# Kernel optimization log

Hardware: AMD Instinct MI355X
Metric: run time of the kernel (lower is better)

## Reference

```python
import jax, jax.numpy as jnp
import numpy as np

D_MODEL = 768
D_STATE = 16
D_CONV = 4
EXPAND = 2
HEADDIM = 64
D_INNER = EXPAND * D_MODEL          # 1536
NHEADS = D_INNER // HEADDIM         # 24
CONV_DIM = D_INNER + 2 * D_STATE    # 1568
D_IN_PROJ = 2 * D_INNER + 2 * D_STATE + NHEADS  # 3128
BATCH, SEQ = 4, 2048


def _mamba_params(key, scale=0.02):
    ks = jax.random.split(key, 5)
    return dict(
        in_w=jax.random.normal(ks[0], (D_MODEL, D_IN_PROJ), jnp.float32) * scale,
        conv_w=jax.random.normal(ks[1], (CONV_DIM, D_CONV), jnp.float32) * scale,
        conv_b=jnp.zeros((CONV_DIM,), jnp.float32),
        dt_bias=jax.random.normal(ks[2], (NHEADS,), jnp.float32) * 0.1,
        A_log=jnp.log(jax.random.uniform(ks[3], (NHEADS,), jnp.float32, 1.0, 16.0)),
        D=jnp.ones((NHEADS,), jnp.float32),
        norm_w=jnp.ones((D_INNER,), jnp.float32),
        out_w=jax.random.normal(ks[4], (D_INNER, D_MODEL), jnp.float32) * scale,
    )


def setup_inputs() -> dict:
    key = jax.random.key(0)
    kx, kf, kb, k1, k2 = jax.random.split(key, 5)
    f = _mamba_params(kf)
    b = _mamba_params(kb)
    k1a, k1b = jax.random.split(k1)
    inp = {
        'x': jax.random.normal(kx, (BATCH, SEQ, D_MODEL), jnp.float32),
        'ln1_w': jnp.ones((D_MODEL,), jnp.float32), 'ln1_b': jnp.zeros((D_MODEL,), jnp.float32),
        'ln2_w': jnp.ones((D_MODEL,), jnp.float32), 'ln2_b': jnp.zeros((D_MODEL,), jnp.float32),
        'ffn_w1': jax.random.normal(k1a, (2 * D_MODEL, 4 * D_MODEL), jnp.float32) * 0.02,
        'ffn_b1': jnp.zeros((4 * D_MODEL,), jnp.float32),
        'ffn_w2': jax.random.normal(k1b, (4 * D_MODEL, D_MODEL), jnp.float32) * 0.02,
        'ffn_b2': jnp.zeros((D_MODEL,), jnp.float32),
    }
    for name, p in (('f', f), ('b', b)):
        for k, v in p.items():
            inp[name + '_' + k] = v
    return inp


def _layernorm(x, w, b, eps=1e-5):
    m = jnp.mean(x, -1, keepdims=True)
    v = jnp.mean((x - m) ** 2, -1, keepdims=True)
    return (x - m) * jax.lax.rsqrt(v + eps) * w + b


def _mamba2(u, in_w, conv_w, conv_b, dt_bias, A_log, D, norm_w, out_w):
    b, l, _ = u.shape
    zxbcdt = u @ in_w                               # (b,l,d_in_proj)
    z = zxbcdt[..., :D_INNER]
    xBC = zxbcdt[..., D_INNER:D_INNER + CONV_DIM]
    dt = jax.nn.softplus(zxbcdt[..., -NHEADS:] + dt_bias)   # (b,l,h)
    # depthwise causal conv1d (kernel D_CONV) + SiLU
    xpad = jnp.pad(xBC, ((0, 0), (D_CONV - 1, 0), (0, 0)))
    xc = sum(conv_w[:, k] * xpad[:, k:k + l, :] for k in range(D_CONV)) + conv_b
    xc = jax.nn.silu(xc)
    xh = xc[..., :D_INNER].reshape(b, l, NHEADS, HEADDIM)
    Bm = xc[..., D_INNER:D_INNER + D_STATE]          # (b,l,n), ngroups=1
    Cm = xc[..., D_INNER + D_STATE:]                 # (b,l,n)
    A = -jnp.exp(A_log)                              # (h,)
    dA = jnp.exp(dt * A)                             # (b,l,h)

    def step(h, inp):
        dA_t, dt_t, B_t, C_t, x_t = inp              # (b,h),(b,h),(b,n),(b,n),(b,h,p)
        h = h * dA_t[:, :, None, None] + (dt_t[:, :, None] * x_t)[..., None] * B_t[:, None, None, :]
        y = jnp.einsum('bhpn,bn->bhp', h, C_t)
        return h, y

    h0 = jnp.zeros((b, NHEADS, HEADDIM, D_STATE), u.dtype)
    xs = (dA.transpose(1, 0, 2), dt.transpose(1, 0, 2), Bm.transpose(1, 0, 2),
          Cm.transpose(1, 0, 2), xh.transpose(1, 0, 2, 3))
    _, ys = jax.lax.scan(step, h0, xs)               # ys: (l,b,h,p)
    y = ys.transpose(1, 0, 2, 3) + D[None, None, :, None] * xh
    y = y.reshape(b, l, D_INNER)
    # gated RMSNorm: rmsnorm(y * silu(z)) * weight
    yz = y * jax.nn.silu(z)
    yz = yz * jax.lax.rsqrt(jnp.mean(yz * yz, -1, keepdims=True) + 1e-5) * norm_w
    return yz @ out_w


def reference(x, ln1_w, ln1_b, ln2_w, ln2_b,
              f_in_w, f_conv_w, f_conv_b, f_dt_bias, f_A_log, f_D, f_norm_w, f_out_w,
              b_in_w, b_conv_w, b_conv_b, b_dt_bias, b_A_log, b_D, b_norm_w, b_out_w,
              ffn_w1, ffn_b1, ffn_w2, ffn_b2):
    xn = _layernorm(x, ln1_w, ln1_b)
    fo = _mamba2(xn, f_in_w, f_conv_w, f_conv_b, f_dt_bias, f_A_log, f_D, f_norm_w, f_out_w)
    bo = _mamba2(jnp.flip(xn, 1), b_in_w, b_conv_w, b_conv_b, b_dt_bias, b_A_log, b_D, b_norm_w, b_out_w)
    bo = jnp.flip(bo, 1)
    bi = jnp.concatenate([fo, bo], -1)
    h = jax.nn.gelu(bi @ ffn_w1 + ffn_b1, approximate=False)
    h = jax.nn.gelu(h @ ffn_w2 + ffn_b2, approximate=False)
    # dropout is identity in eval mode
    return _layernorm(x + h, ln2_w, ln2_b)
```

## Files before the change

### kernel.cpp

```cpp
#include <hip/hip_runtime.h>
#include <math.h>

#define BATCH   4
#define SEQ     2048
#define DMODEL  768
#define DSTATE  16
#define DCONV   4
#define HEADDIM 64
#define DINNER  1536
#define NHEADS  24
#define CONVDIM 1568
#define DINPROJ 3128
#define DFFN    3072
#define ROWS    (BATCH*SEQ)
#define QCH     128
#define NCHUNK  (SEQ/QCH)

typedef __attribute__((ext_vector_type(8))) short bhalf8;
typedef __attribute__((ext_vector_type(4))) float floatx4;

__device__ __forceinline__ float gelu_f(float x) {
    return 0.5f * x * (1.0f + erff(x * 0.70710678118654752f));
}

__device__ __forceinline__ void splitRNE(float v, unsigned short& h, unsigned short& l) {
    unsigned u = __float_as_uint(v);
    unsigned rr = u + 0x7FFFu + ((u >> 16) & 1u);
    unsigned short hi = (unsigned short)(rr >> 16);
    float rem = v - __uint_as_float(((unsigned)hi) << 16);
    unsigned u2 = __float_as_uint(rem);
    unsigned r2 = u2 + 0x7FFFu + ((u2 >> 16) & 1u);
    h = hi;
    l = (unsigned short)(r2 >> 16);
}

__device__ __forceinline__ void gl16(const unsigned short* g, unsigned short* l) {
    __builtin_amdgcn_global_load_lds(
        (const __attribute__((address_space(1))) void*)g,
        (__attribute__((address_space(3))) void*)l, 16, 0, 0);
}

__device__ __forceinline__ float2 blockReduce2(float a, float b) {
    #pragma unroll
    for (int o = 32; o > 0; o >>= 1) {
        a += __shfl_down(a, o, 64);
        b += __shfl_down(b, o, 64);
    }
    __shared__ float sa[4], sb[4];
    int w = threadIdx.x >> 6, lane = threadIdx.x & 63;
    if (lane == 0) { sa[w] = a; sb[w] = b; }
    __syncthreads();
    if (threadIdx.x == 0) {
        int nw = blockDim.x >> 6;
        for (int i = 1; i < nw; ++i) { a += sa[i]; b += sb[i]; }
        sa[0] = a; sb[0] = b;
    }
    __syncthreads();
    return make_float2(sa[0], sb[0]);
}

__global__ __launch_bounds__(256) void ln_kernel(
    const float* __restrict__ x, const float* __restrict__ res,
    const float* __restrict__ w, const float* __restrict__ b,
    float* __restrict__ out)
{
    int r = blockIdx.x;
    const float* xr = x + (size_t)r * DMODEL;
    float v[3]; float s = 0.f, ss = 0.f;
    #pragma unroll
    for (int i = 0; i < 3; ++i) {
        int c = threadIdx.x + i * 256;
        float t = xr[c];
        if (res) t += res[(size_t)r * DMODEL + c];
        v[i] = t; s += t; ss += t * t;
    }
    float2 red = blockReduce2(s, ss);
    float mean = red.x * (1.0f / DMODEL);
    float var  = red.y * (1.0f / DMODEL) - mean * mean;
    float inv  = rsqrtf(var + 1e-5f);
    #pragma unroll
    for (int i = 0; i < 3; ++i) {
        int c = threadIdx.x + i * 256;
        out[(size_t)r * DMODEL + c] = (v[i] - mean) * inv * w[c] + b[c];
    }
}

__global__ __launch_bounds__(256) void ln_split_kernel(
    const float* __restrict__ x,
    const float* __restrict__ w, const float* __restrict__ b,
    unsigned short* __restrict__ H, unsigned short* __restrict__ L)
{
    int r = blockIdx.x;
    const float* xr = x + (size_t)r * DMODEL;
    float v[3]; float s = 0.f, ss = 0.f;
    #pragma unroll
    for (int i = 0; i < 3; ++i) {
        int c = threadIdx.x + i * 256;
        float t = xr[c];
        v[i] = t; s += t; ss += t * t;
    }
    float2 red = blockReduce2(s, ss);
    float mean = red.x * (1.0f / DMODEL);
    float var  = red.y * (1.0f / DMODEL) - mean * mean;
    float inv  = rsqrtf(var + 1e-5f);
    #pragma unroll
    for (int i = 0; i < 3; ++i) {
        int c = threadIdx.x + i * 256;
        float o = (v[i] - mean) * inv * w[c] + b[c];
        unsigned short h, l;
        splitRNE(o, h, l);
        H[(size_t)r * DMODEL + c] = h;
        L[(size_t)r * DMODEL + c] = l;
    }
}

__global__ __launch_bounds__(256) void wconv(
    const float* __restrict__ W, unsigned short* __restrict__ TH,
    unsigned short* __restrict__ TL, int K, int N)
{
    __shared__ float t[32][33];
    int tx = threadIdx.x & 31, ty = threadIdx.x >> 5;
    int kb = blockIdx.y * 32, nb = blockIdx.x * 32;
    #pragma unroll
    for (int i = 0; i < 4; ++i) {
        int k = kb + ty + i * 8, n = nb + tx;
        t[ty + i * 8][tx] = (k < K && n < N) ? W[(size_t)k * N + n] : 0.f;
    }
    __syncthreads();
    #pragma unroll
    for (int i = 0; i < 4; ++i) {
        int n = nb + ty + i * 8, k = kb + tx;
        if (n < N && k < K) {
            unsigned short hi, lo;
            splitRNE(t[tx][ty + i * 8], hi, lo);
            TH[(size_t)n * K + k] = hi;
            TL[(size_t)n * K + k] = lo;
        }
    }
}

__global__ __launch_bounds__(256) void gemm3(
    const unsigned short* __restrict__ AHg, const unsigned short* __restrict__ ALg,
    const unsigned short* __restrict__ BHg, const unsigned short* __restrict__ BLg,
    float* __restrict__ C, unsigned short* __restrict__ CHo, unsigned short* __restrict__ CLo,
    const float* __restrict__ bias,
    int M, int N, int K, int ldc, int coloff,
    int revA, int revC, int act)
{
    (void)M;
    __shared__ __align__(16) unsigned short AsH[128 * 32], AsL[128 * 32];
    __shared__ __align__(16) unsigned short BsH[128 * 32], BsL[128 * 32];

    const int tid = threadIdx.x;
    const int m0 = blockIdx.y * 128;
    const int n0 = blockIdx.x * 128;

    size_t aoff[2], boff[2];
    int lofs[2];
    #pragma unroll
    for (int q = 0; q < 2; ++q) {
        int row = (tid >> 2) + 64 * q;
        int sd  = (tid & 3) ^ ((row >> 1) & 3);
        int ar = m0 + row;
        if (revA) ar = (ar & ~(SEQ - 1)) + (SEQ - 1 - (ar & (SEQ - 1)));
        aoff[q] = (size_t)ar * K + sd * 8;
        boff[q] = (size_t)(n0 + row) * K + sd * 8;
        lofs[q] = (tid + 256 * q) * 8;
    }

    auto stage = [&](int k0) {
        #pragma unroll
        for (int q = 0; q < 2; ++q) {
            gl16(AHg + aoff[q] + k0, AsH + lofs[q]);
            gl16(ALg + aoff[q] + k0, AsL + lofs[q]);
            gl16(BHg + boff[q] + k0, BsH + lofs[q]);
            gl16(BLg + boff[q] + k0, BsL + lofs[q]);
        }
    };

    auto frag = [&](const unsigned short* buf, int row, int slot) -> bhalf8 {
        int sp = slot ^ ((row >> 1) & 3);
        return *(const bhalf8*)(buf + row * 32 + sp * 8);
    };

    const int w = tid >> 6, lane = tid & 63;
    const int rw = (w >> 1) * 64, cw = (w & 1) * 64;
    const int lr = lane & 15;
    const int lq = lane >> 4;

    floatx4 acc[4][4];
    const floatx4 fz = {0.f, 0.f, 0.f, 0.f};
    #pragma unroll
    for (int i = 0; i < 4; ++i)
        #pragma unroll
        for (int j = 0; j < 4; ++j) acc[i][j] = fz;

    const int ktiles = K >> 5;
    stage(0);
    for (int kt = 0; kt < ktiles; ++kt) {
        __syncthreads();
        bhalf8 ah[4], al[4], bh[4], bl[4];
        #pragma unroll
        for (int i = 0; i < 4; ++i) {
            int ra = rw + i * 16 + lr;
            int rb = cw + i * 16 + lr;
            ah[i] = frag(AsH, ra, lq);
            al[i] = frag(AsL, ra, lq);
            bh[i] = frag(BsH, rb, lq);
            bl[i] = frag(BsL, rb, lq);
        }
        __syncthreads();
        if (kt + 1 < ktiles) stage((kt + 1) * 32);
        #pragma unroll
        for (int i = 0; i < 4; ++i)
            #pragma unroll
            for (int j = 0; j < 4; ++j) {
                acc[i][j] = __builtin_amdgcn_mfma_f32_16x16x32_bf16(ah[i], bh[j], acc[i][j], 0, 0, 0);
                acc[i][j] = __builtin_amdgcn_mfma_f32_16x16x32_bf16(ah[i], bl[j], acc[i][j], 0, 0, 0);
                acc[i][j] = __builtin_amdgcn_mfma_f32_16x16x32_bf16(al[i], bh[j], acc[i][j], 0, 0, 0);
            }
    }

    #pragma unroll
    for (int i = 0; i < 4; ++i) {
        #pragma unroll
        for (int j = 0; j < 4; ++j) {
            int gc = n0 + cw + j * 16 + lr;
            if (gc < N) {
                float bv = bias ? bias[gc] : 0.f;
                #pragma unroll
                for (int rg = 0; rg < 4; ++rg) {
                    int gm = m0 + rw + i * 16 + lq * 4 + rg;
                    if (revC) gm = (gm & ~(SEQ - 1)) + (SEQ - 1 - (gm & (SEQ - 1)));
                    float v = acc[i][j][rg] + bv;
                    if (act) v = gelu_f(v);
                    size_t o = (size_t)gm * ldc + coloff + gc;
                    if (CHo) {
                        unsigned short h, l;
                        splitRNE(v, h, l);
                        CHo[o] = h; CLo[o] = l;
                    } else {
                        C[o] = v;
                    }
                }
            }
        }
    }
}

__global__ __launch_bounds__(256) void conv_kernel(
    const float* __restrict__ zx, const float* __restrict__ cw,
    const float* __restrict__ cb, float* __restrict__ xcv,
    float* __restrict__ bc,
    const float* __restrict__ dt_bias, const float* __restrict__ A_log,
    float* __restrict__ dtda)
{
    int cg = blockIdx.x * 256 + threadIdx.x;
    int r = blockIdx.y;
    if (cg < CONVDIM / 4) {
        int c = cg * 4;
        int t = r & (SEQ - 1);
        int rb = r & ~(SEQ - 1);
        float4 acc = *(const float4*)&cb[c];
        #pragma unroll
        for (int k = 0; k < DCONV; ++k) {
            int tt = t - (DCONV - 1) + k;
            if (tt >= 0) {
                float4 xv = *(const float4*)&zx[(size_t)(rb + tt) * DINPROJ + DINNER + c];
                acc.x += cw[(c + 0) * DCONV + k] * xv.x;
                acc.y += cw[(c + 1) * DCONV + k] * xv.y;
                acc.z += cw[(c + 2) * DCONV + k] * xv.z;
                acc.w += cw[(c + 3) * DCONV + k] * xv.w;
            }
        }
        float4 v;
        v.x = acc.x / (1.0f + expf(-acc.x));
        v.y = acc.y / (1.0f + expf(-acc.y));
        v.z = acc.z / (1.0f + expf(-acc.z));
        v.w = acc.w / (1.0f + expf(-acc.w));
        if (c < DINNER) *(float4*)&xcv[(size_t)r * DINNER + c] = v;
        else            *(float4*)&bc[(size_t)r * 32 + (c - DINNER)] = v;
    } else if (cg >= CONVDIM / 4 && cg < CONVDIM / 4 + NHEADS / 4) {
        int h0 = (cg - CONVDIM / 4) * 4;
        float4 zv = *(const float4*)&zx[(size_t)r * DINPROJ + (DINPROJ - NHEADS) + h0];
        float zz[4] = {zv.x, zv.y, zv.z, zv.w};
        #pragma unroll
        for (int j = 0; j < 4; ++j) {
            int h = h0 + j;
            float v = zz[j] + dt_bias[h];
            float dt = (v > 20.f) ? v : log1pf(expf(v));
            float A = -expf(A_log[h]);
            float2 o = make_float2(dt, expf(dt * A));
            *(float2*)&dtda[(size_t)r * 48 + 2 * h] = o;
        }
    }
}

__global__ __launch_bounds__(64) void scan_a(
    const float* __restrict__ xcv, const float* __restrict__ bc,
    const float* __restrict__ dtda, const float* __restrict__ Dp,
    float* __restrict__ yout, float* __restrict__ S, float* __restrict__ cd)
{
    int blk = blockIdx.x;
    int bh = blk / NCHUNK, c = blk - bh * NCHUNK;
    int b = bh / NHEADS, h = bh - b * NHEADS;
    int p = threadIdx.x;
    float hs[DSTATE] = {};
    float Dv = Dp[h];
    float cum = 1.f;
    int t0 = c * QCH;
    for (int t = t0; t < t0 + QCH; ++t) {
        size_t r = (size_t)b * SEQ + t;
        float2 dd = *(const float2*)&dtda[r * 48 + 2 * h];
        float dt = dd.x;
        float dA = dd.y;
        float x  = xcv[r * DINNER + h * HEADDIM + p];
        cum *= dA;
        float coef = dt * x;
        const float* bcr = bc + r * 32;
        float y = 0.f;
        #pragma unroll
        for (int n = 0; n < DSTATE; ++n) {
            hs[n] = hs[n] * dA + coef * bcr[n];
            y += hs[n] * bcr[16 + n];
        }
        yout[r * DINPROJ + DINNER + h * HEADDIM + p] = y + Dv * x;
        if (p == 0) cd[r * NHEADS + h] = cum;
    }
    float* Sp = S + (((size_t)bh * NCHUNK + c) * HEADDIM + p) * DSTATE;
    #pragma unroll
    for (int n = 0; n < DSTATE; ++n) Sp[n] = hs[n];
}

__global__ __launch_bounds__(64) void scan_b(
    const float* __restrict__ cd, float* __restrict__ S)
{
    int bh = blockIdx.x;
    int b = bh / NHEADS, h = bh - b * NHEADS;
    int p = threadIdx.x;
    float H[DSTATE] = {};
    for (int c = 0; c < NCHUNK; ++c) {
        float* Sp = S + (((size_t)bh * NCHUNK + c) * HEADDIM + p) * DSTATE;
        float P = cd[((size_t)b * SEQ + c * QCH + QCH - 1) * NHEADS + h];
        float s[DSTATE];
        #pragma unroll
        for (int n = 0; n < DSTATE; ++n) s[n] = Sp[n];
        #pragma unroll
        for (int n = 0; n < DSTATE; ++n) Sp[n] = H[n];
        #pragma unroll
        for (int n = 0; n < DSTATE; ++n) H[n] = P * H[n] + s[n];
    }
}

__global__ __launch_bounds__(64) void scan_c(
    const float* __restrict__ bc, const float* __restrict__ cd,
    const float* __restrict__ S, float* __restrict__ yout)
{
    int blk = blockIdx.x;
    int bh = blk / (NCHUNK - 1), c = blk - bh * (NCHUNK - 1) + 1;
    int b = bh / NHEADS, h = bh - b * NHEADS;
    int p = threadIdx.x;
    const float* Hp = S + (((size_t)bh * NCHUNK + c) * HEADDIM + p) * DSTATE;
    float H[DSTATE];
    #pragma unroll
    for (int n = 0; n < DSTATE; ++n) H[n] = Hp[n];
    int t0 = c * QCH;
    for (int t = t0; t < t0 + QCH; ++t) {
        size_t r = (size_t)b * SEQ + t;
        const float* Cr = bc + r * 32 + 16;
        float dot = 0.f;
        #pragma unroll
        for (int n = 0; n < DSTATE; ++n) dot += H[n] * Cr[n];
        float cum = cd[r * NHEADS + h];
        yout[r * DINPROJ + DINNER + h * HEADDIM + p] += cum * dot;
    }
}

__global__ __launch_bounds__(256) void gnorm_kernel(
    const float* __restrict__ zx, const float* __restrict__ nw,
    unsigned short* __restrict__ H, unsigned short* __restrict__ L)
{
    int r = blockIdx.x;
    const float* zr = zx + (size_t)r * DINPROJ;
    float v[6]; float ss = 0.f;
    #pragma unroll
    for (int i = 0; i < 6; ++i) {
        int c = threadIdx.x + i * 256;
        float z = zr[c];
        float y = zr[DINNER + c];
        float t = y * z / (1.0f + expf(-z));
        v[i] = t; ss += t * t;
    }
    float2 red = blockReduce2(ss, 0.f);
    float sc = rsqrtf(red.x * (1.0f / DINNER) + 1e-5f);
    #pragma unroll
    for (int i = 0; i < 6; ++i) {
        int c = threadIdx.x + i * 256;
        float o = v[i] * sc * nw[c];
        unsigned short h, l;
        splitRNE(o, h, l);
        H[(size_t)r * DINNER + c] = h;
        L[(size_t)r * DINNER + c] = l;
    }
}

extern "C" void kernel_launch(void* const* d_in, const int* in_sizes, int n_in,
                              void* d_out, int out_size, void* d_ws, size_t ws_size,
                              hipStream_t stream)
{
    (void)in_sizes; (void)n_in; (void)out_size; (void)ws_size;
    const float* x     = (const float*)d_in[0];
    const float* ln1w  = (const float*)d_in[1];
    const float* ln1b  = (const float*)d_in[2];
    const float* ln2w  = (const float*)d_in[3];
    const float* ln2b  = (const float*)d_in[4];
    const float* ffnw1 = (const float*)d_in[5];
    const float* ffnb1 = (const float*)d_in[6];
    const float* ffnw2 = (const float*)d_in[7];
    const float* ffnb2 = (const float*)d_in[8];
    const float* p[2][8];
    for (int d = 0; d < 2; ++d)
        for (int i = 0; i < 8; ++i)
            p[d][i] = (const float*)d_in[9 + d * 8 + i];

    float* ws   = (float*)d_ws;
    float* zx   = ws;
    float* bi   = zx + (size_t)ROWS * DINPROJ;
    float* S    = bi + (size_t)ROWS * DINNER;
    float* Wbuf = S  + (size_t)ROWS * DINNER;
    float* bcb  = Wbuf + 2402304;
    float* dtda = bcb + (size_t)ROWS * 32;
    float* Sbuf = Wbuf;
    float* cdbf = Wbuf + (size_t)BATCH * NHEADS * NCHUNK * HEADDIM * DSTATE;

    unsigned short* xnH = (unsigned short*)d_out;
    unsigned short* xnL = xnH + (size_t)ROWS * DMODEL;
    float* xcv = S;
    unsigned short* znH = (unsigned short*)S;
    unsigned short* znL = znH + (size_t)ROWS * DINNER;
    unsigned short* biH = (unsigned short*)bi;
    unsigned short* biL = biH + (size_t)ROWS * DINNER;
    unsigned short* hmH = (unsigned short*)zx;
    unsigned short* hmL = hmH + (size_t)ROWS * DFFN;
    float* ffo = S + 4718592;

    ln_split_kernel<<<ROWS, 256, 0, stream>>>(x, ln1w, ln1b, xnH, xnL);

    for (int d = 0; d < 2; ++d) {
        unsigned short* WH = (unsigned short*)Wbuf;
        unsigned short* WL = WH + (size_t)DINPROJ * DMODEL;
        wconv<<<dim3((DINPROJ + 31) / 32, DMODEL / 32), 256, 0, stream>>>(
            p[d][0], WH, WL, DMODEL, DINPROJ);
        gemm3<<<dim3((DINPROJ + 127) / 128, ROWS / 128), 256, 0, stream>>>(
            xnH, xnL, WH, WL, zx, nullptr, nullptr, nullptr,
            ROWS, DINPROJ, DMODEL, DINPROJ, 0, d, 0, 0);
        conv_kernel<<<dim3(2, ROWS), 256, 0, stream>>>(
            zx, p[d][1], p[d][2], xcv, bcb, p[d][3], p[d][4], dtda);
        scan_a<<<BATCH * NHEADS * NCHUNK, 64, 0, stream>>>(
            xcv, bcb, dtda, p[d][5], zx, Sbuf, cdbf);
        scan_b<<<BATCH * NHEADS, 64, 0, stream>>>(cdbf, Sbuf);
        scan_c<<<BATCH * NHEADS * (NCHUNK - 1), 64, 0, stream>>>(
            bcb, cdbf, Sbuf, zx);
        gnorm_kernel<<<ROWS, 256, 0, stream>>>(zx, p[d][6], znH, znL);
        unsigned short* WL2 = WH + (size_t)DMODEL * DINNER;
        wconv<<<dim3(DMODEL / 32, DINNER / 32), 256, 0, stream>>>(
            p[d][7], WH, WL2, DINNER, DMODEL);
        gemm3<<<dim3(DMODEL / 128, ROWS / 128), 256, 0, stream>>>(
            znH, znL, WH, WL2, nullptr, biH, biL, nullptr,
            ROWS, DMODEL, DINNER, DINNER, d * DMODEL, 0, d, 0);
    }

    {
        unsigned short* WH = (unsigned short*)S;
        unsigned short* WL = WH + (size_t)DFFN * DINNER;
        wconv<<<dim3(DFFN / 32, DINNER / 32), 256, 0, stream>>>(
            ffnw1, WH, WL, DINNER, DFFN);
        gemm3<<<dim3(DFFN / 128, ROWS / 128), 256, 0, stream>>>(
            biH, biL, WH, WL, nullptr, hmH, hmL, ffnb1,
            ROWS, DFFN, DINNER, DFFN, 0, 0, 0, 1);
    }
    {
        unsigned short* WH = (unsigned short*)S;
        unsigned short* WL = WH + (size_t)DMODEL * DFFN;
        wconv<<<dim3(DMODEL / 32, DFFN / 32), 256, 0, stream>>>(
            ffnw2, WH, WL, DFFN, DMODEL);
        gemm3<<<dim3(DMODEL / 128, ROWS / 128), 256, 0, stream>>>(
            hmH, hmL, WH, WL, ffo, nullptr, nullptr, ffnb2,
            ROWS, DMODEL, DFFN, DMODEL, 0, 0, 0, 1);
    }
    ln_kernel<<<ROWS, 256, 0, stream>>>(x, ffo, ln2w, ln2b, (float*)d_out);
}
```

Before: 1.563 ms.

## Add single-wave 64x64 GEMM kernel for narrow-N out-proj and FFN2 GEMMs

```diff
diff --git a/kernel.cpp b/kernel.cpp
--- a/kernel.cpp
+++ b/kernel.cpp
@@ -248,6 +248,112 @@
     }
 }
 
+__global__ __launch_bounds__(64) void gemm1w(
+    const unsigned short* __restrict__ AHg, const unsigned short* __restrict__ ALg,
+    const unsigned short* __restrict__ BHg, const unsigned short* __restrict__ BLg,
+    float* __restrict__ C, unsigned short* __restrict__ CHo, unsigned short* __restrict__ CLo,
+    const float* __restrict__ bias,
+    int M, int N, int K, int ldc, int coloff,
+    int revA, int revC, int act)
+{
+    (void)M;
+    __shared__ __align__(16) unsigned short AsH[64 * 32], AsL[64 * 32];
+    __shared__ __align__(16) unsigned short BsH[64 * 32], BsL[64 * 32];
+
+    const int tid = threadIdx.x;
+    const int m0 = blockIdx.y * 64;
+    const int n0 = blockIdx.x * 64;
+
+    size_t aoff[4], boff[4];
+    int lofs[4];
+    #pragma unroll
+    for (int q = 0; q < 4; ++q) {
+        int row = (tid >> 2) + 16 * q;
+        int sd  = (tid & 3) ^ ((row >> 1) & 3);
+        int ar = m0 + row;
+        if (revA) ar = (ar & ~(SEQ - 1)) + (SEQ - 1 - (ar & (SEQ - 1)));
+        aoff[q] = (size_t)ar * K + sd * 8;
+        boff[q] = (size_t)(n0 + row) * K + sd * 8;
+        lofs[q] = (tid + 64 * q) * 8;
+    }
+
+    auto stage = [&](int k0) {
+        #pragma unroll
+        for (int q = 0; q < 4; ++q) {
+            gl16(AHg + aoff[q] + k0, AsH + lofs[q]);
+            gl16(ALg + aoff[q] + k0, AsL + lofs[q]);
+            gl16(BHg + boff[q] + k0, BsH + lofs[q]);
+            gl16(BLg + boff[q] + k0, BsL + lofs[q]);
+        }
+    };
+
+    auto frag = [&](const unsigned short* buf, int row, int slot) -> bhalf8 {
+        int sp = slot ^ ((row >> 1) & 3);
+        return *(const bhalf8*)(buf + row * 32 + sp * 8);
+    };
+
+    const int lr = tid & 15;
+    const int lq = tid >> 4;
+
+    floatx4 acc[4][4];
+    const floatx4 fz = {0.f, 0.f, 0.f, 0.f};
+    #pragma unroll
+    for (int i = 0; i < 4; ++i)
+        #pragma unroll
+        for (int j = 0; j < 4; ++j) acc[i][j] = fz;
+
+    const int ktiles = K >> 5;
+    stage(0);
+    for (int kt = 0; kt < ktiles; ++kt) {
+        asm volatile("s_waitcnt vmcnt(0)" ::: "memory");
+        bhalf8 ah[4], al[4], bh[4], bl[4];
+        #pragma unroll
+        for (int i = 0; i < 4; ++i) {
+            int rr = i * 16 + lr;
+            ah[i] = frag(AsH, rr, lq);
+            al[i] = frag(AsL, rr, lq);
+            bh[i] = frag(BsH, rr, lq);
+            bl[i] = frag(BsL, rr, lq);
+        }
+        asm volatile("s_waitcnt lgkmcnt(0)" ::: "memory");
+        if (kt + 1 < ktiles) stage((kt + 1) * 32);
+        #pragma unroll
+        for (int i = 0; i < 4; ++i)
+            #pragma unroll
+            for (int j = 0; j < 4; ++j) {
+                acc[i][j] = __builtin_amdgcn_mfma_f32_16x16x32_bf16(ah[i], bh[j], acc[i][j], 0, 0, 0);
+                acc[i][j] = __builtin_amdgcn_mfma_f32_16x16x32_bf16(ah[i], bl[j], acc[i][j], 0, 0, 0);
+                acc[i][j] = __builtin_amdgcn_mfma_f32_16x16x32_bf16(al[i], bh[j], acc[i][j], 0, 0, 0);
+            }
+    }
+
+    #pragma unroll
+    for (int i = 0; i < 4; ++i) {
+        #pragma unroll
+        for (int j = 0; j < 4; ++j) {
+            int gc = n0 + j * 16 + lr;
+            if (gc < N) {
+                float bv = bias ? bias[gc] : 0.f;
+                #pragma unroll
+                for (int rg = 0; rg < 4; ++rg) {
+                    int gm = m0 + i * 16 + lq * 4 + rg;
+                    if (revC) gm = (gm & ~(SEQ - 1)) + (SEQ - 1 - (gm & (SEQ - 1)));
+                    float v = acc[i][j][rg] + bv;
+                    if (act) v = gelu_f(v);
+                    size_t o = (size_t)gm * ldc + coloff + gc;
+                    if (CHo) {
+                        unsigned short h, l;
+                        splitRNE(v, h, l);
+                        CHo[o] = h; CLo[o] = l;
+                    } else {
+                        C[o] = v;
+                    }
+                }
+            }
+        }
+    }
+}
+
 __global__ __launch_bounds__(256) void conv_kernel(
     const float* __restrict__ zx, const float* __restrict__ cw,
     const float* __restrict__ cb, float* __restrict__ xcv,
@@ -465,7 +571,7 @@
         unsigned short* WL2 = WH + (size_t)DMODEL * DINNER;
         wconv<<<dim3(DMODEL / 32, DINNER / 32), 256, 0, stream>>>(
             p[d][7], WH, WL2, DINNER, DMODEL);
-        gemm3<<<dim3(DMODEL / 128, ROWS / 128), 256, 0, stream>>>(
+        gemm1w<<<dim3(DMODEL / 64, ROWS / 64), 64, 0, stream>>>(
             znH, znL, WH, WL2, nullptr, biH, biL, nullptr,
             ROWS, DMODEL, DINNER, DINNER, d * DMODEL, 0, d, 0);
     }
@@ -484,7 +590,7 @@
         unsigned short* WL = WH + (size_t)DMODEL * DFFN;
         wconv<<<dim3(DMODEL / 32, DFFN / 32), 256, 0, stream>>>(
             ffnw2, WH, WL, DFFN, DMODEL);
-        gemm3<<<dim3(DMODEL / 128, ROWS / 128), 256, 0, stream>>>(
+        gemm1w<<<dim3(DMODEL / 64, ROWS / 64), 64, 0, stream>>>(
             hmH, hmL, WH, WL, ffo, nullptr, nullptr, ffnb2,
             ROWS, DMODEL, DFFN, DMODEL, 0, 0, 0, 1);
     }
```

New measurement: 1.712 ms. 1.1x slower.
